# Kernel tuning notes

Hardware: AMD Instinct MI355X
Metric: run time of the kernel (lower is better)

The kernel has to match this reference:

```python
import jax, jax.numpy as jnp
import numpy as np

N = 100000      # nodes
E = 1200000     # edges (avg degree 12)
DIN = 64        # input_dim
HID = 64        # hidden_dim
HEADS = 4
CH = HID // 4   # 16 per-head channels; concat -> HID


def setup_inputs() -> dict:
    key = jax.random.key(0)
    ks = jax.random.split(key, 16)
    s = 0.05
    return {
        "x": jax.random.normal(ks[0], (N, DIN), jnp.float32),
        "edge_index": jax.random.randint(ks[1], (2, E), 0, N, jnp.int32),
        # GCN layers
        "W1": s * jax.random.normal(ks[2], (DIN, HID), jnp.float32),
        "b1": jnp.zeros((HID,), jnp.float32),
        "W2": s * jax.random.normal(ks[3], (HID, HID), jnp.float32),
        "b2": jnp.zeros((HID,), jnp.float32),
        "W3": s * jax.random.normal(ks[4], (HID, HID // 2), jnp.float32),
        "b3": jnp.zeros((HID // 2,), jnp.float32),
        # GAT layer: in = HID//2 = 32, out per head = HID//4 = 16, 4 heads concat -> 64
        "Wg": s * jax.random.normal(ks[5], (HID // 2, HEADS * CH), jnp.float32),
        "att_src": s * jax.random.normal(ks[6], (HEADS, CH), jnp.float32),
        "att_dst": s * jax.random.normal(ks[7], (HEADS, CH), jnp.float32),
        "bg": jnp.zeros((HEADS * CH,), jnp.float32),
        # classifier MLP
        "Wc1": s * jax.random.normal(ks[8], (HID, HID // 2), jnp.float32),
        "bc1": jnp.zeros((HID // 2,), jnp.float32),
        "Wc2": s * jax.random.normal(ks[9], (HID // 2, 2), jnp.float32),
        "bc2": jnp.zeros((2,), jnp.float32),
    }


def reference(x, edge_index, W1, b1, W2, b2, W3, b3,
              Wg, att_src, att_dst, bg, Wc1, bc1, Wc2, bc2):
    n = x.shape[0]
    # add self-loops (PyG default for GCNConv and GATConv)
    loops = jnp.arange(n, dtype=edge_index.dtype)
    src = jnp.concatenate([edge_index[0], loops])
    dst = jnp.concatenate([edge_index[1], loops])

    # symmetric GCN normalization: deg^-1/2[src] * deg^-1/2[dst]
    deg = jax.ops.segment_sum(jnp.ones(src.shape, x.dtype), dst, num_segments=n)
    dinv = jnp.where(deg > 0, jax.lax.rsqrt(deg), 0.0)
    norm = (dinv[src] * dinv[dst])[:, None]  # [E+N, 1]

    def gcn(h, W, b):
        h = h @ W                                   # [N, out]
        msg = h[src] * norm                         # gather + scale, [E+N, out]
        return jax.ops.segment_sum(msg, dst, num_segments=n) + b

    h = jax.nn.relu(gcn(x, W1, b1))   # dropout = identity (eval mode)
    h = jax.nn.relu(gcn(h, W2, b2))
    h = jax.nn.relu(gcn(h, W3, b3))   # [N, HID//2]

    # GATConv, 4 heads, concat
    heads, ch = att_src.shape
    g = (h @ Wg).reshape(n, heads, ch)                       # [N, H, C]
    a_s = jnp.einsum('nhc,hc->nh', g, att_src)               # [N, H]
    a_d = jnp.einsum('nhc,hc->nh', g, att_dst)
    e = jax.nn.leaky_relu(a_s[src] + a_d[dst], 0.2)          # [E+N, H]
    m = jax.ops.segment_max(e, dst, num_segments=n)          # per-dst max
    ex = jnp.exp(e - m[dst])
    den = jax.ops.segment_sum(ex, dst, num_segments=n)
    alpha = ex / den[dst]                                    # segment softmax
    o = jax.ops.segment_sum(g[src] * alpha[:, :, None], dst, num_segments=n)
    o = jax.nn.relu(o.reshape(n, heads * ch) + bg)           # [N, HID]

    pooled = jnp.mean(o, axis=0, keepdims=True)              # batch=None path: [1, HID]
    z = jax.nn.relu(pooled @ Wc1 + bc1)
    return z @ Wc2 + bc2                                     # [1, 2]
```

## Files before the change

kernel.cpp:

```cpp
#include <hip/hip_runtime.h>
#include <hip/hip_bf16.h>
#include <hip/hip_fp16.h>
#include <math.h>

__device__ __forceinline__ unsigned h2u(__half2 h) { return *reinterpret_cast<unsigned*>(&h); }
__device__ __forceinline__ __half2 u2h(unsigned u) { return *reinterpret_cast<__half2*>(&u); }
__device__ __forceinline__ __half2 shfl_h2(__half2 h, int off) {
  int v = __shfl_xor((int)h2u(h), off);
  unsigned uv = (unsigned)v;
  return u2h(uv);
}


#define P1E 16
#define NBK 400

__global__ __launch_bounds__(256) void hist_gemm1(const int* __restrict__ dst,
                                                  int* __restrict__ bcnt, int e,
                                                  int fillBlocks,
                                                  const float* __restrict__ H,
                                                  const float* __restrict__ W,
                                                  unsigned short* __restrict__ T, int n) {
  __shared__ int lcnt[NBK];
  __shared__ float Ws[64 * 64];
  if ((int)blockIdx.x < fillBlocks) {
    for (int i = threadIdx.x; i < NBK; i += 256) lcnt[i] = 0;
    __syncthreads();
    int base = blockIdx.x * (256 * P1E);
#pragma unroll
    for (int r = 0; r < P1E; ++r) {
      int i = base + r * 256 + threadIdx.x;
      if (i < e) atomicAdd(&lcnt[dst[i] >> 8], 1);
    }
    __syncthreads();
    for (int b = threadIdx.x; b < NBK; b += 256)
      if (lcnt[b]) atomicAdd(&bcnt[b], lcnt[b]);
    return;
  }
  for (int idx = threadIdx.x; idx < 64 * 64 / 4; idx += 256)
    reinterpret_cast<float4*>(Ws)[idx] = reinterpret_cast<const float4*>(W)[idx];
  __syncthreads();
  int bid = blockIdx.x - fillBlocks;
  int tx = threadIdx.x % 16;
  int ty = threadIdx.x / 16;
  int j0 = tx * 4;
  int n0 = bid * 32 + ty * 2;
  const float* h0p = H + (size_t)min(n0 + 0, n - 1) * 64;
  const float* h1p = H + (size_t)min(n0 + 1, n - 1) * 64;
  float4 acc0 = {0,0,0,0}, acc1 = {0,0,0,0};
#pragma unroll 2
  for (int k = 0; k < 64; k += 4) {
    float4 ha = *reinterpret_cast<const float4*>(h0p + k);
    float4 hb = *reinterpret_cast<const float4*>(h1p + k);
    float4 w0 = *reinterpret_cast<const float4*>(&Ws[(k + 0) * 64 + j0]);
    float4 w1 = *reinterpret_cast<const float4*>(&Ws[(k + 1) * 64 + j0]);
    float4 w2 = *reinterpret_cast<const float4*>(&Ws[(k + 2) * 64 + j0]);
    float4 w3 = *reinterpret_cast<const float4*>(&Ws[(k + 3) * 64 + j0]);
#define A4(A, HV)                                                                \
    A.x = fmaf(HV.x, w0.x, A.x); A.y = fmaf(HV.x, w0.y, A.y);                    \
    A.z = fmaf(HV.x, w0.z, A.z); A.w = fmaf(HV.x, w0.w, A.w);                    \
    A.x = fmaf(HV.y, w1.x, A.x); A.y = fmaf(HV.y, w1.y, A.y);                    \
    A.z = fmaf(HV.y, w1.z, A.z); A.w = fmaf(HV.y, w1.w, A.w);                    \
    A.x = fmaf(HV.z, w2.x, A.x); A.y = fmaf(HV.z, w2.y, A.y);                    \
    A.z = fmaf(HV.z, w2.z, A.z); A.w = fmaf(HV.z, w2.w, A.w);                    \
    A.x = fmaf(HV.w, w3.x, A.x); A.y = fmaf(HV.w, w3.y, A.y);                    \
    A.z = fmaf(HV.w, w3.z, A.z); A.w = fmaf(HV.w, w3.w, A.w);
    A4(acc0, ha) A4(acc1, hb)
#undef A4
  }
  float4 av[2] = {acc0, acc1};
#pragma unroll
  for (int i = 0; i < 2; ++i) {
    int node = n0 + i;
    if (node < n) {
      uint2 st;
      st.x = h2u(__floats2half2_rn(av[i].x, av[i].y));
      st.y = h2u(__floats2half2_rn(av[i].z, av[i].w));
      *reinterpret_cast<uint2*>(T + (size_t)node * 64 + j0) = st;
    }
  }
}

__global__ __launch_bounds__(512) void bucket_scan(const int* __restrict__ bcnt,
                                                   int* __restrict__ bucket_base,
                                                   int* __restrict__ gcursor,
                                                   int nb, int e) {
  __shared__ int s[512];
  int v = (threadIdx.x < (unsigned)nb) ? bcnt[threadIdx.x] : 0;
  s[threadIdx.x] = v;
  __syncthreads();
  for (int off = 1; off < 512; off <<= 1) {
    int t = (threadIdx.x >= (unsigned)off) ? s[threadIdx.x - off] : 0;
    __syncthreads();
    s[threadIdx.x] += t;
    __syncthreads();
  }
  if (threadIdx.x < (unsigned)nb) {
    int excl = s[threadIdx.x] - v;
    bucket_base[threadIdx.x] = excl;
    gcursor[threadIdx.x] = excl;
  }
  if (threadIdx.x == 0) bucket_base[nb] = e;
}

__global__ __launch_bounds__(256) void bin_pass1(const int* __restrict__ src,
                                                 const int* __restrict__ dst,
                                                 int* __restrict__ gcursor,
                                                 unsigned* __restrict__ stream, int e) {
  __shared__ int lcnt[NBK], gbase[NBK];
  for (int i = threadIdx.x; i < NBK; i += 256) lcnt[i] = 0;
  __syncthreads();
  int base = blockIdx.x * (256 * P1E);
  int rankr[P1E];
#pragma unroll
  for (int r = 0; r < P1E; ++r) {
    int i = base + r * 256 + threadIdx.x;
    rankr[r] = (i < e) ? atomicAdd(&lcnt[dst[i] >> 8], 1) : 0;
  }
  __syncthreads();
  for (int bkt = threadIdx.x; bkt < NBK; bkt += 256)
    gbase[bkt] = lcnt[bkt] ? atomicAdd(&gcursor[bkt], lcnt[bkt]) : 0;
  __syncthreads();
#pragma unroll
  for (int r = 0; r < P1E; ++r) {
    int i = base + r * 256 + threadIdx.x;
    if (i < e) {
      int d = dst[i];
      stream[gbase[d >> 8] + rankr[r]] = ((unsigned)src[i] << 8) | (unsigned)(d & 255);
    }
  }
}


#define LCAP 6144

__global__ __launch_bounds__(256) void bin_pass2(const unsigned* __restrict__ stream,
                                                 const int* __restrict__ bucket_base,
                                                 int* __restrict__ row_start,
                                                 int* __restrict__ cnt,
                                                 int* __restrict__ csr_src,
                                                 int n, int e) {
  __shared__ int lcnt[256];
  __shared__ int lscan[256];
  __shared__ int lcur[256];
  __shared__ int lbuf[LCAP];
  int node_lo = blockIdx.x << 8;
  int nn = min(256, n - node_lo);
  int lo = bucket_base[blockIdx.x];
  int hi = bucket_base[blockIdx.x + 1];
  int sz = hi - lo;
  lcnt[threadIdx.x] = 0;
  __syncthreads();
  for (int j = threadIdx.x; j < sz; j += 256)
    atomicAdd(&lcnt[stream[lo + j] & 255], 1);
  __syncthreads();
  int v = lcnt[threadIdx.x];
  lscan[threadIdx.x] = v;
  __syncthreads();
  for (int off = 1; off < 256; off <<= 1) {
    int t = (threadIdx.x >= (unsigned)off) ? lscan[threadIdx.x - off] : 0;
    __syncthreads();
    lscan[threadIdx.x] += t;
    __syncthreads();
  }
  int excl = lscan[threadIdx.x] - v;
  if ((int)threadIdx.x < nn) {
    row_start[node_lo + threadIdx.x] = lo + excl;
    cnt[node_lo + threadIdx.x] = v;
  }
  if (blockIdx.x == 0 && threadIdx.x == 0) row_start[n] = e;
  lcur[threadIdx.x] = excl;
  __syncthreads();
  if (sz <= LCAP) {
    for (int j = threadIdx.x; j < sz; j += 256) {
      unsigned r = stream[lo + j];
      int slot = atomicAdd(&lcur[r & 255], 1);
      lbuf[slot] = (int)(r >> 8);
    }
    __syncthreads();
    for (int j = threadIdx.x; j < sz; j += 256)
      csr_src[lo + j] = lbuf[j];
  } else {
    for (int j = threadIdx.x; j < sz; j += 256) {
      unsigned r = stream[lo + j];
      int slot = atomicAdd(&lcur[r & 255], 1);
      csr_src[lo + slot] = (int)(r >> 8);
    }
  }
}


template <int IN, int OUT, bool ATT>
__global__ __launch_bounds__(256) void gemm2x4(const unsigned short* __restrict__ Hh,
                                               const float* __restrict__ W,
                                               const float* __restrict__ att_src,
                                               const float* __restrict__ att_dst,
                                               unsigned short* __restrict__ T,
                                               float* __restrict__ a_s,
                                               float* __restrict__ a_d, int n) {
  constexpr int TX = OUT / 4;
  constexpr int NB = (256 / TX) * 2;
  __shared__ float Ws[IN * OUT];
  __shared__ float asv[ATT ? OUT : 1], adv[ATT ? OUT : 1];
  __shared__ float lds_as[ATT ? NB * 4 : 1], lds_ad[ATT ? NB * 4 : 1];

  for (int idx = threadIdx.x; idx < IN * OUT / 4; idx += 256)
    reinterpret_cast<float4*>(Ws)[idx] = reinterpret_cast<const float4*>(W)[idx];
  if (ATT) {
    if (threadIdx.x < OUT) {
      asv[threadIdx.x] = att_src[threadIdx.x];
      adv[threadIdx.x] = att_dst[threadIdx.x];
    }
    for (int idx = threadIdx.x; idx < NB * 4; idx += 256) {
      lds_as[idx] = 0.f; lds_ad[idx] = 0.f;
    }
  }
  __syncthreads();

  int tx = threadIdx.x % TX;
  int ty = threadIdx.x / TX;
  int j0 = tx * 4;
  int base = blockIdx.x * NB;
  int n0 = base + ty * 2;

  const unsigned short* h0p = Hh + (size_t)min(n0 + 0, n - 1) * IN;
  const unsigned short* h1p = Hh + (size_t)min(n0 + 1, n - 1) * IN;

  float4 acc0 = {0,0,0,0}, acc1 = {0,0,0,0};
#pragma unroll 2
  for (int k = 0; k < IN; k += 4) {
    uint2 va = *reinterpret_cast<const uint2*>(h0p + k);
    uint2 vb = *reinterpret_cast<const uint2*>(h1p + k);
    float2 a01 = __half22float2(u2h(va.x)), a23 = __half22float2(u2h(va.y));
    float2 b01 = __half22float2(u2h(vb.x)), b23 = __half22float2(u2h(vb.y));
    float4 ha = {a01.x, a01.y, a23.x, a23.y};
    float4 hb = {b01.x, b01.y, b23.x, b23.y};
    float4 w0 = *reinterpret_cast<const float4*>(&Ws[(k + 0) * OUT + j0]);
    float4 w1 = *reinterpret_cast<const float4*>(&Ws[(k + 1) * OUT + j0]);
    float4 w2 = *reinterpret_cast<const float4*>(&Ws[(k + 2) * OUT + j0]);
    float4 w3 = *reinterpret_cast<const float4*>(&Ws[(k + 3) * OUT + j0]);
#define A4(A, HV)                                                                \
    A.x = fmaf(HV.x, w0.x, A.x); A.y = fmaf(HV.x, w0.y, A.y);                    \
    A.z = fmaf(HV.x, w0.z, A.z); A.w = fmaf(HV.x, w0.w, A.w);                    \
    A.x = fmaf(HV.y, w1.x, A.x); A.y = fmaf(HV.y, w1.y, A.y);                    \
    A.z = fmaf(HV.y, w1.z, A.z); A.w = fmaf(HV.y, w1.w, A.w);                    \
    A.x = fmaf(HV.z, w2.x, A.x); A.y = fmaf(HV.z, w2.y, A.y);                    \
    A.z = fmaf(HV.z, w2.z, A.z); A.w = fmaf(HV.z, w2.w, A.w);                    \
    A.x = fmaf(HV.w, w3.x, A.x); A.y = fmaf(HV.w, w3.y, A.y);                    \
    A.z = fmaf(HV.w, w3.z, A.z); A.w = fmaf(HV.w, w3.w, A.w);
    A4(acc0, ha) A4(acc1, hb)
#undef A4
  }

  float4 av[2] = {acc0, acc1};
#pragma unroll
  for (int i = 0; i < 2; ++i) {
    int node = n0 + i;
    if (node < n) {
      float o0 = av[i].x, o1 = av[i].y, o2 = av[i].z, o3 = av[i].w;
      uint2 st;
      st.x = h2u(__floats2half2_rn(o0, o1));
      st.y = h2u(__floats2half2_rn(o2, o3));
      *reinterpret_cast<uint2*>(T + (size_t)node * OUT + j0) = st;
      if (ATT) {
        int head = tx >> 2;
        float cs = o0 * asv[j0] + o1 * asv[j0 + 1] + o2 * asv[j0 + 2] + o3 * asv[j0 + 3];
        float cd = o0 * adv[j0] + o1 * adv[j0 + 1] + o2 * adv[j0 + 2] + o3 * adv[j0 + 3];
        atomicAdd(&lds_as[(ty * 2 + i) * 4 + head], cs);
        atomicAdd(&lds_ad[(ty * 2 + i) * 4 + head], cd);
      }
    }
  }
  if (ATT) {
    __syncthreads();
    for (int idx = threadIdx.x; idx < NB * 4; idx += 256) {
      int node = base + (idx >> 2);
      if (node < n) {
        a_s[(size_t)base * 4 + idx] = lds_as[idx];
        a_d[(size_t)base * 4 + idx] = lds_ad[idx];
      }
    }
  }
}


template <int C, bool DINV, bool PRE>
__global__ __launch_bounds__(256) void gcn_agg(const unsigned short* __restrict__ T,
                                               const int* __restrict__ row_start,
                                               const int* __restrict__ csr_src,
                                               const int* __restrict__ cnt,
                                               const float* __restrict__ b,
                                               unsigned short* __restrict__ out, int n) {
  constexpr int LPR = C / 8;
  constexpr int SLOTS = 64 / LPR;
  constexpr unsigned RS4 = C / 8;
  int wid = threadIdx.x >> 6;
  int lane = threadIdx.x & 63;
  int node = blockIdx.x * 4 + wid;
  if (node >= n) return;
  int q = lane & (LPR - 1);
  int g = lane / LPR;
  const uint4* Tp = reinterpret_cast<const uint4*>(T);
  int rs = row_start[node], re = row_start[node + 1];
  float dn = rsqrtf((float)(cnt[node] + 1));
  __half2 A0 = u2h(0u), A1 = u2h(0u), A2 = u2h(0u), A3 = u2h(0u);
  if (g == 0) {
    uint4 v = Tp[(unsigned)node * RS4 + q];
    if constexpr (DINV) {
      __half2 hw = __float2half2_rn(dn);
      A0 = __hmul2(hw, u2h(v.x)); A1 = __hmul2(hw, u2h(v.y));
      A2 = __hmul2(hw, u2h(v.z)); A3 = __hmul2(hw, u2h(v.w));
    } else {
      A0 = u2h(v.x); A1 = u2h(v.y); A2 = u2h(v.z); A3 = u2h(v.w);
    }
  }
  if constexpr (C == 64) {
    __half2 B0 = u2h(0u), B1 = u2h(0u), B2 = u2h(0u), B3 = u2h(0u);
    int i = rs + g;
    while (i < re) {
      bool v2 = (i + 8) < re;
      unsigned s1 = (unsigned)csr_src[i];
      unsigned s2 = v2 ? (unsigned)csr_src[i + 8] : s1;
      uint4 r1 = Tp[s1 * RS4 + q];
      uint4 r2 = Tp[s2 * RS4 + q];
      if constexpr (DINV) {
        float w1f = rsqrtf((float)(cnt[s1] + 1));
        float w2f = v2 ? rsqrtf((float)(cnt[s2] + 1)) : 0.f;
        __half2 hw1 = __float2half2_rn(w1f);
        __half2 hw2 = __float2half2_rn(w2f);
        A0 = __hfma2(hw1, u2h(r1.x), A0); A1 = __hfma2(hw1, u2h(r1.y), A1);
        A2 = __hfma2(hw1, u2h(r1.z), A2); A3 = __hfma2(hw1, u2h(r1.w), A3);
        B0 = __hfma2(hw2, u2h(r2.x), B0); B1 = __hfma2(hw2, u2h(r2.y), B1);
        B2 = __hfma2(hw2, u2h(r2.z), B2); B3 = __hfma2(hw2, u2h(r2.w), B3);
      } else {
        if (!v2) { r2.x = 0u; r2.y = 0u; r2.z = 0u; r2.w = 0u; }
        A0 = __hadd2(A0, u2h(r1.x)); A1 = __hadd2(A1, u2h(r1.y));
        A2 = __hadd2(A2, u2h(r1.z)); A3 = __hadd2(A3, u2h(r1.w));
        B0 = __hadd2(B0, u2h(r2.x)); B1 = __hadd2(B1, u2h(r2.y));
        B2 = __hadd2(B2, u2h(r2.z)); B3 = __hadd2(B3, u2h(r2.w));
      }
      i += 16;
    }
    A0 = __hadd2(A0, B0); A1 = __hadd2(A1, B1);
    A2 = __hadd2(A2, B2); A3 = __hadd2(A3, B3);
  } else {
    for (int i = rs + g; i < re; i += SLOTS) {
      unsigned s = (unsigned)csr_src[i];
      uint4 v = Tp[s * RS4 + q];
      A0 = __hadd2(A0, u2h(v.x)); A1 = __hadd2(A1, u2h(v.y));
      A2 = __hadd2(A2, u2h(v.z)); A3 = __hadd2(A3, u2h(v.w));
    }
  }
#pragma unroll
  for (int off = LPR; off < 64; off <<= 1) {
    A0 = __hadd2(A0, shfl_h2(A0, off));
    A1 = __hadd2(A1, shfl_h2(A1, off));
    A2 = __hadd2(A2, shfl_h2(A2, off));
    A3 = __hadd2(A3, shfl_h2(A3, off));
  }
  if (lane < LPR) {
    float4 b0 = *reinterpret_cast<const float4*>(b + 8 * q);
    float4 b1 = *reinterpret_cast<const float4*>(b + 8 * q + 4);
    float2 f0 = __half22float2(A0), f1 = __half22float2(A1);
    float2 f2 = __half22float2(A2), f3 = __half22float2(A3);
    float sc = PRE ? dn : 1.f;
    float r0 = sc * fmaxf(fmaf(dn, f0.x, b0.x), 0.f);
    float r1 = sc * fmaxf(fmaf(dn, f0.y, b0.y), 0.f);
    float r2 = sc * fmaxf(fmaf(dn, f1.x, b0.z), 0.f);
    float r3 = sc * fmaxf(fmaf(dn, f1.y, b0.w), 0.f);
    float r4 = sc * fmaxf(fmaf(dn, f2.x, b1.x), 0.f);
    float r5 = sc * fmaxf(fmaf(dn, f2.y, b1.y), 0.f);
    float r6 = sc * fmaxf(fmaf(dn, f3.x, b1.z), 0.f);
    float r7 = sc * fmaxf(fmaf(dn, f3.y, b1.w), 0.f);
    uint4 o;
    o.x = h2u(__floats2half2_rn(r0, r1));
    o.y = h2u(__floats2half2_rn(r2, r3));
    o.z = h2u(__floats2half2_rn(r4, r5));
    o.w = h2u(__floats2half2_rn(r6, r7));
    reinterpret_cast<uint4*>(out)[(unsigned)node * RS4 + q] = o;
  }
}


__device__ __forceinline__ float lrelu(float v) { return v > 0.f ? v : 0.2f * v; }

__global__ __launch_bounds__(256) void gat_agg(const unsigned short* __restrict__ g,
                                               const float* __restrict__ a_s,
                                               const float* __restrict__ a_d,
                                               const int* __restrict__ row_start,
                                               const int* __restrict__ csr_src,
                                               const float* __restrict__ bg,
                                               float* __restrict__ partial1, int n) {
  __shared__ float pacc[4][64];
  int wid = threadIdx.x >> 6;
  int lane = threadIdx.x & 63;
  int node = blockIdx.x * 4 + wid;
  bool active = node < n;
  int q = lane & 7;
  int gslot = lane >> 3;
  int h = q >> 1;
  const uint4* gp = reinterpret_cast<const uint4*>(g);
  int rs = 0, re = 0;
  float ad_h = 0.f;
  if (active) {
    rs = row_start[node];
    re = row_start[node + 1];
    ad_h = a_d[(unsigned)node * 4u + h];
  }
  float den = 0.f, den2 = 0.f;
  __half2 A0 = u2h(0u), A1 = u2h(0u), A2 = u2h(0u), A3 = u2h(0u);
  __half2 C0 = u2h(0u), C1 = u2h(0u), C2 = u2h(0u), C3 = u2h(0u);
  if (active && gslot == 0) {
    float w = __expf(lrelu(a_s[(unsigned)node * 4u + h] + ad_h));
    uint4 v = gp[(unsigned)node * 8u + q];
    den = w;
    __half2 w2 = __float2half2_rn(w);
    A0 = __hmul2(w2, u2h(v.x)); A1 = __hmul2(w2, u2h(v.y));
    A2 = __hmul2(w2, u2h(v.z)); A3 = __hmul2(w2, u2h(v.w));
  }
  int i = rs + gslot;
  while (i < re) {
    bool v2 = (i + 8) < re;
    unsigned s1 = (unsigned)csr_src[i];
    unsigned s2 = v2 ? (unsigned)csr_src[i + 8] : s1;
    float e1 = a_s[s1 * 4u + h];
    float e2 = a_s[s2 * 4u + h];
    uint4 r1 = gp[s1 * 8u + q];
    uint4 r2 = gp[s2 * 8u + q];
    float w1 = __expf(lrelu(e1 + ad_h));
    float w2 = v2 ? __expf(lrelu(e2 + ad_h)) : 0.f;
    den += w1;
    den2 += w2;
    __half2 hw1 = __float2half2_rn(w1);
    __half2 hw2 = __float2half2_rn(w2);
    A0 = __hfma2(hw1, u2h(r1.x), A0); A1 = __hfma2(hw1, u2h(r1.y), A1);
    A2 = __hfma2(hw1, u2h(r1.z), A2); A3 = __hfma2(hw1, u2h(r1.w), A3);
    C0 = __hfma2(hw2, u2h(r2.x), C0); C1 = __hfma2(hw2, u2h(r2.y), C1);
    C2 = __hfma2(hw2, u2h(r2.z), C2); C3 = __hfma2(hw2, u2h(r2.w), C3);
    i += 16;
  }
  den += den2;
  A0 = __hadd2(A0, C0); A1 = __hadd2(A1, C1);
  A2 = __hadd2(A2, C2); A3 = __hadd2(A3, C3);
#pragma unroll
  for (int off = 8; off < 64; off <<= 1) {
    den += __shfl_xor(den, off);
    A0 = __hadd2(A0, shfl_h2(A0, off));
    A1 = __hadd2(A1, shfl_h2(A1, off));
    A2 = __hadd2(A2, shfl_h2(A2, off));
    A3 = __hadd2(A3, shfl_h2(A3, off));
  }
  if (lane < 8) {
    float inv = active ? (1.f / den) : 0.f;
    float4 b0 = *reinterpret_cast<const float4*>(bg + 8 * q);
    float4 b1 = *reinterpret_cast<const float4*>(bg + 8 * q + 4);
    float2 f0 = __half22float2(A0), f1 = __half22float2(A1);
    float2 f2 = __half22float2(A2), f3 = __half22float2(A3);
    int c0 = 8 * q;
    pacc[wid][c0 + 0] = active ? fmaxf(fmaf(f0.x, inv, b0.x), 0.f) : 0.f;
    pacc[wid][c0 + 1] = active ? fmaxf(fmaf(f0.y, inv, b0.y), 0.f) : 0.f;
    pacc[wid][c0 + 2] = active ? fmaxf(fmaf(f1.x, inv, b0.z), 0.f) : 0.f;
    pacc[wid][c0 + 3] = active ? fmaxf(fmaf(f1.y, inv, b0.w), 0.f) : 0.f;
    pacc[wid][c0 + 4] = active ? fmaxf(fmaf(f2.x, inv, b1.x), 0.f) : 0.f;
    pacc[wid][c0 + 5] = active ? fmaxf(fmaf(f2.y, inv, b1.y), 0.f) : 0.f;
    pacc[wid][c0 + 6] = active ? fmaxf(fmaf(f3.x, inv, b1.z), 0.f) : 0.f;
    pacc[wid][c0 + 7] = active ? fmaxf(fmaf(f3.y, inv, b1.w), 0.f) : 0.f;
  }
  __syncthreads();
  if (threadIdx.x < 64) {
    int t = threadIdx.x;
    partial1[(size_t)blockIdx.x * 64 + t] =
        pacc[0][t] + pacc[1][t] + pacc[2][t] + pacc[3][t];
  }
}


#define PBLK 512

__global__ __launch_bounds__(256) void pool_partial(const float* __restrict__ P1,
                                                    double* __restrict__ partial2,
                                                    unsigned total) {
  unsigned tid = blockIdx.x * 256u + threadIdx.x;
  unsigned stride = PBLK * 256u;
  double a = 0.0;
  for (unsigned i = tid; i < total; i += stride) a += (double)P1[i];
  __shared__ double red[256];
  red[threadIdx.x] = a;
  __syncthreads();
  if (threadIdx.x < 64) {
    int t = threadIdx.x;
    double s = red[t] + red[t + 64] + red[t + 128] + red[t + 192];
    partial2[(size_t)blockIdx.x * 64 + t] = s;
  }
}

__global__ __launch_bounds__(64) void final_kernel(const double* __restrict__ partial, int nblocks,
                                                   const float* __restrict__ Wc1,
                                                   const float* __restrict__ bc1,
                                                   const float* __restrict__ Wc2,
                                                   const float* __restrict__ bc2,
                                                   float* __restrict__ out, int n) {
  __shared__ float pooled[64];
  __shared__ float z[32];
  int t = threadIdx.x;
  double s = 0.0;
#pragma unroll 4
  for (int b = 0; b < nblocks; ++b) s += partial[(size_t)b * 64 + t];
  pooled[t] = (float)(s / (double)n);
  __syncthreads();
  if (t < 32) {
    double a = 0.0;
    for (int k = 0; k < 64; ++k) a += (double)pooled[k] * (double)Wc1[k * 32 + t];
    z[t] = fmaxf((float)a + bc1[t], 0.f);
  }
  __syncthreads();
  if (t < 2) {
    double a = 0.0;
    for (int j = 0; j < 32; ++j) a += (double)z[j] * (double)Wc2[j * 2 + t];
    out[t] = (float)a + bc2[t];
  }
}


extern "C" void kernel_launch(void* const* d_in, const int* in_sizes, int n_in,
                              void* d_out, int out_size, void* d_ws, size_t ws_size,
                              hipStream_t stream) {
  const float* x   = (const float*)d_in[0];
  const int* eidx  = (const int*)d_in[1];
  const float* W1  = (const float*)d_in[2];
  const float* b1  = (const float*)d_in[3];
  const float* W2  = (const float*)d_in[4];
  const float* b2  = (const float*)d_in[5];
  const float* W3  = (const float*)d_in[6];
  const float* b3  = (const float*)d_in[7];
  const float* Wg  = (const float*)d_in[8];
  const float* att_src = (const float*)d_in[9];
  const float* att_dst = (const float*)d_in[10];
  const float* bg  = (const float*)d_in[11];
  const float* Wc1 = (const float*)d_in[12];
  const float* bc1 = (const float*)d_in[13];
  const float* Wc2 = (const float*)d_in[14];
  const float* bc2 = (const float*)d_in[15];

  const int n = in_sizes[0] / 64;
  const int e = in_sizes[1] / 2;
  const int* src = eidx;
  const int* dst = eidx + e;

  char* ws = (char*)d_ws;
  size_t off = 0;
  auto alloc = [&](size_t bytes) {
    void* p = ws + off;
    off += (bytes + 255) & ~(size_t)255;
    return p;
  };
  const int nbuckets = (n + 255) >> 8;
  const int nblk4 = (n + 3) / 4;
  int*      cnt        = (int*)alloc((size_t)n * 4);
  int*      row_start  = (int*)alloc(((size_t)n + 1) * 4);
  unsigned* stream_b   = (unsigned*)alloc((size_t)e * 4);
  int*      csr_src    = (int*)alloc((size_t)e * 4);
  int*      bcnt       = (int*)alloc(NBK * 4);
  int*      bucket_base = (int*)alloc((NBK + 1) * 4);
  int*      gcursor    = (int*)alloc(NBK * 4);
  unsigned short* bufT = (unsigned short*)alloc((size_t)n * 64 * 2);
  unsigned short* bufF = (unsigned short*)alloc((size_t)n * 64 * 2);
  float*    a_s        = (float*)alloc((size_t)n * 4 * 4);
  float*    a_d        = (float*)alloc((size_t)n * 4 * 4);
  float*    partial1   = (float*)alloc((size_t)nblk4 * 64 * 4);
  double*   partial2   = (double*)alloc((size_t)PBLK * 64 * 8);

  hipMemsetAsync(bcnt, 0, NBK * 4, stream);

  int g64 = (n + 31) / 32;
  int g32 = (n + 63) / 64;
  int p1blk = (e + 256 * P1E - 1) / (256 * P1E);

  hist_gemm1<<<p1blk + g64, 256, 0, stream>>>(dst, bcnt, e, p1blk, x, W1, bufT, n);
  bucket_scan<<<1, 512, 0, stream>>>(bcnt, bucket_base, gcursor, nbuckets, e);
  bin_pass1<<<p1blk, 256, 0, stream>>>(src, dst, gcursor, stream_b, e);
  bin_pass2<<<nbuckets, 256, 0, stream>>>(stream_b, bucket_base, row_start, cnt,
                                          csr_src, n, e);

  gcn_agg<64, true, true><<<nblk4, 256, 0, stream>>>(bufT, row_start, csr_src, cnt, b1, bufF, n);
  gemm2x4<64, 64, false><<<g64, 256, 0, stream>>>(bufF, W2, nullptr, nullptr,
                                                  bufT, nullptr, nullptr, n);
  gcn_agg<64, false, true><<<nblk4, 256, 0, stream>>>(bufT, row_start, csr_src, cnt, b2, bufF, n);
  gemm2x4<64, 32, false><<<g32, 256, 0, stream>>>(bufF, W3, nullptr, nullptr,
                                                  bufT, nullptr, nullptr, n);
  gcn_agg<32, false, false><<<nblk4, 256, 0, stream>>>(bufT, row_start, csr_src, cnt, b3, bufF, n);
  gemm2x4<32, 64, true><<<g64, 256, 0, stream>>>(bufF, Wg, att_src, att_dst,
                                                 bufT, a_s, a_d, n);
  gat_agg<<<nblk4, 256, 0, stream>>>(bufT, a_s, a_d, row_start, csr_src, bg, partial1, n);
  pool_partial<<<PBLK, 256, 0, stream>>>(partial1, partial2, (unsigned)nblk4 * 64u);
  final_kernel<<<1, 64, 0, stream>>>(partial2, PBLK, Wc1, bc1, Wc2, bc2, (float*)d_out, n);
}
```

Measured before the change: 315.6 us.

## Fuse GCN aggregation with following dense GEMM in one kernel

Merges each gcn_agg pass with the next layer's weight multiply (and the GAT attention-score computation) into one 1024-thread kernel. Each block aggregates 16 nodes into shared memory, then multiplies by the weight matrix held in shared memory. This removes three launches and the round trip of the aggregated features through global memory. In exchange, each block reloads the full weight matrix, uses a scalar per-output GEMM, and the larger blocks may lower occupancy.

```diff
diff --git a/kernel.cpp b/kernel.cpp
--- a/kernel.cpp
+++ b/kernel.cpp
@@ -131,7 +131,6 @@
   }
 }
 
-
 #define LCAP 6144
 
 __global__ __launch_bounds__(256) void bin_pass2(const unsigned* __restrict__ stream,
@@ -190,121 +189,51 @@
 }
 
 
-template <int IN, int OUT, bool ATT>
-__global__ __launch_bounds__(256) void gemm2x4(const unsigned short* __restrict__ Hh,
-                                               const float* __restrict__ W,
-                                               const float* __restrict__ att_src,
-                                               const float* __restrict__ att_dst,
-                                               unsigned short* __restrict__ T,
-                                               float* __restrict__ a_s,
-                                               float* __restrict__ a_d, int n) {
-  constexpr int TX = OUT / 4;
-  constexpr int NB = (256 / TX) * 2;
-  __shared__ float Ws[IN * OUT];
-  __shared__ float asv[ATT ? OUT : 1], adv[ATT ? OUT : 1];
-  __shared__ float lds_as[ATT ? NB * 4 : 1], lds_ad[ATT ? NB * 4 : 1];
-
-  for (int idx = threadIdx.x; idx < IN * OUT / 4; idx += 256)
+__device__ __forceinline__ float lrelu(float v) { return v > 0.f ? v : 0.2f * v; }
+
+template <int CIN, int COUT, bool DINV, bool ATT, bool SCO>
+__global__ __launch_bounds__(1024) void gcn_gemm(const unsigned short* __restrict__ T,
+                                                 const int* __restrict__ row_start,
+                                                 const int* __restrict__ csr_src,
+                                                 const int* __restrict__ cnt,
+                                                 const float* __restrict__ b,
+                                                 const float* __restrict__ W,
+                                                 const float* __restrict__ att_src,
+                                                 const float* __restrict__ att_dst,
+                                                 unsigned short* __restrict__ Tout,
+                                                 float* __restrict__ a_s,
+                                                 float* __restrict__ a_d, int n) {
+  constexpr int LPR = CIN / 8;
+  constexpr unsigned RS4 = CIN / 8;
+  __shared__ float Ws[CIN * COUT];
+  __shared__ float hrow[16][CIN];
+  __shared__ float asv[ATT ? COUT : 1], adv[ATT ? COUT : 1];
+
+  for (int idx = threadIdx.x; idx < CIN * COUT / 4; idx += 1024)
     reinterpret_cast<float4*>(Ws)[idx] = reinterpret_cast<const float4*>(W)[idx];
   if (ATT) {
-    if (threadIdx.x < OUT) {
+    if (threadIdx.x < COUT) {
       asv[threadIdx.x] = att_src[threadIdx.x];
       adv[threadIdx.x] = att_dst[threadIdx.x];
     }
-    for (int idx = threadIdx.x; idx < NB * 4; idx += 256) {
-      lds_as[idx] = 0.f; lds_ad[idx] = 0.f;
-    }
-  }
-  __syncthreads();
-
-  int tx = threadIdx.x % TX;
-  int ty = threadIdx.x / TX;
-  int j0 = tx * 4;
-  int base = blockIdx.x * NB;
-  int n0 = base + ty * 2;
-
-  const unsigned short* h0p = Hh + (size_t)min(n0 + 0, n - 1) * IN;
-  const unsigned short* h1p = Hh + (size_t)min(n0 + 1, n - 1) * IN;
-
-  float4 acc0 = {0,0,0,0}, acc1 = {0,0,0,0};
-#pragma unroll 2
-  for (int k = 0; k < IN; k += 4) {
-    uint2 va = *reinterpret_cast<const uint2*>(h0p + k);
-    uint2 vb = *reinterpret_cast<const uint2*>(h1p + k);
-    float2 a01 = __half22float2(u2h(va.x)), a23 = __half22float2(u2h(va.y));
-    float2 b01 = __half22float2(u2h(vb.x)), b23 = __half22float2(u2h(vb.y));
-    float4 ha = {a01.x, a01.y, a23.x, a23.y};
-    float4 hb = {b01.x, b01.y, b23.x, b23.y};
-    float4 w0 = *reinterpret_cast<const float4*>(&Ws[(k + 0) * OUT + j0]);
-    float4 w1 = *reinterpret_cast<const float4*>(&Ws[(k + 1) * OUT + j0]);
-    float4 w2 = *reinterpret_cast<const float4*>(&Ws[(k + 2) * OUT + j0]);
-    float4 w3 = *reinterpret_cast<const float4*>(&Ws[(k + 3) * OUT + j0]);
-#define A4(A, HV)                                                                \
-    A.x = fmaf(HV.x, w0.x, A.x); A.y = fmaf(HV.x, w0.y, A.y);                    \
-    A.z = fmaf(HV.x, w0.z, A.z); A.w = fmaf(HV.x, w0.w, A.w);                    \
-    A.x = fmaf(HV.y, w1.x, A.x); A.y = fmaf(HV.y, w1.y, A.y);                    \
-    A.z = fmaf(HV.y, w1.z, A.z); A.w = fmaf(HV.y, w1.w, A.w);                    \
-    A.x = fmaf(HV.z, w2.x, A.x); A.y = fmaf(HV.z, w2.y, A.y);                    \
-    A.z = fmaf(HV.z, w2.z, A.z); A.w = fmaf(HV.z, w2.w, A.w);                    \
-    A.x = fmaf(HV.w, w3.x, A.x); A.y = fmaf(HV.w, w3.y, A.y);                    \
-    A.z = fmaf(HV.w, w3.z, A.z); A.w = fmaf(HV.w, w3.w, A.w);
-    A4(acc0, ha) A4(acc1, hb)
-#undef A4
-  }
-
-  float4 av[2] = {acc0, acc1};
-#pragma unroll
-  for (int i = 0; i < 2; ++i) {
-    int node = n0 + i;
-    if (node < n) {
-      float o0 = av[i].x, o1 = av[i].y, o2 = av[i].z, o3 = av[i].w;
-      uint2 st;
-      st.x = h2u(__floats2half2_rn(o0, o1));
-      st.y = h2u(__floats2half2_rn(o2, o3));
-      *reinterpret_cast<uint2*>(T + (size_t)node * OUT + j0) = st;
-      if (ATT) {
-        int head = tx >> 2;
-        float cs = o0 * asv[j0] + o1 * asv[j0 + 1] + o2 * asv[j0 + 2] + o3 * asv[j0 + 3];
-        float cd = o0 * adv[j0] + o1 * adv[j0 + 1] + o2 * adv[j0 + 2] + o3 * adv[j0 + 3];
-        atomicAdd(&lds_as[(ty * 2 + i) * 4 + head], cs);
-        atomicAdd(&lds_ad[(ty * 2 + i) * 4 + head], cd);
-      }
-    }
-  }
-  if (ATT) {
-    __syncthreads();
-    for (int idx = threadIdx.x; idx < NB * 4; idx += 256) {
-      int node = base + (idx >> 2);
-      if (node < n) {
-        a_s[(size_t)base * 4 + idx] = lds_as[idx];
-        a_d[(size_t)base * 4 + idx] = lds_ad[idx];
-      }
-    }
-  }
-}
-
-
-template <int C, bool DINV, bool PRE>
-__global__ __launch_bounds__(256) void gcn_agg(const unsigned short* __restrict__ T,
-                                               const int* __restrict__ row_start,
-                                               const int* __restrict__ csr_src,
-                                               const int* __restrict__ cnt,
-                                               const float* __restrict__ b,
-                                               unsigned short* __restrict__ out, int n) {
-  constexpr int LPR = C / 8;
-  constexpr int SLOTS = 64 / LPR;
-  constexpr unsigned RS4 = C / 8;
+  }
+
   int wid = threadIdx.x >> 6;
   int lane = threadIdx.x & 63;
-  int node = blockIdx.x * 4 + wid;
-  if (node >= n) return;
+  int node = blockIdx.x * 16 + wid;
+  bool active = node < n;
   int q = lane & (LPR - 1);
   int g = lane / LPR;
   const uint4* Tp = reinterpret_cast<const uint4*>(T);
-  int rs = row_start[node], re = row_start[node + 1];
-  float dn = rsqrtf((float)(cnt[node] + 1));
+  int rs = 0, re = 0;
+  float dn = 1.f;
+  if (active) {
+    rs = row_start[node];
+    re = row_start[node + 1];
+    dn = rsqrtf((float)(cnt[node] + 1));
+  }
   __half2 A0 = u2h(0u), A1 = u2h(0u), A2 = u2h(0u), A3 = u2h(0u);
-  if (g == 0) {
+  if (active && g == 0) {
     uint4 v = Tp[(unsigned)node * RS4 + q];
     if constexpr (DINV) {
       __half2 hw = __float2half2_rn(dn);
@@ -314,7 +243,7 @@
       A0 = u2h(v.x); A1 = u2h(v.y); A2 = u2h(v.z); A3 = u2h(v.w);
     }
   }
-  if constexpr (C == 64) {
+  if constexpr (CIN == 64) {
     __half2 B0 = u2h(0u), B1 = u2h(0u), B2 = u2h(0u), B3 = u2h(0u);
     int i = rs + g;
     while (i < re) {
@@ -344,7 +273,7 @@
     A0 = __hadd2(A0, B0); A1 = __hadd2(A1, B1);
     A2 = __hadd2(A2, B2); A3 = __hadd2(A3, B3);
   } else {
-    for (int i = rs + g; i < re; i += SLOTS) {
+    for (int i = rs + g; i < re; i += 16) {
       unsigned s = (unsigned)csr_src[i];
       uint4 v = Tp[s * RS4 + q];
       A0 = __hadd2(A0, u2h(v.x)); A1 = __hadd2(A1, u2h(v.y));
@@ -363,26 +292,56 @@
     float4 b1 = *reinterpret_cast<const float4*>(b + 8 * q + 4);
     float2 f0 = __half22float2(A0), f1 = __half22float2(A1);
     float2 f2 = __half22float2(A2), f3 = __half22float2(A3);
-    float sc = PRE ? dn : 1.f;
-    float r0 = sc * fmaxf(fmaf(dn, f0.x, b0.x), 0.f);
-    float r1 = sc * fmaxf(fmaf(dn, f0.y, b0.y), 0.f);
-    float r2 = sc * fmaxf(fmaf(dn, f1.x, b0.z), 0.f);
-    float r3 = sc * fmaxf(fmaf(dn, f1.y, b0.w), 0.f);
-    float r4 = sc * fmaxf(fmaf(dn, f2.x, b1.x), 0.f);
-    float r5 = sc * fmaxf(fmaf(dn, f2.y, b1.y), 0.f);
-    float r6 = sc * fmaxf(fmaf(dn, f3.x, b1.z), 0.f);
-    float r7 = sc * fmaxf(fmaf(dn, f3.y, b1.w), 0.f);
-    uint4 o;
-    o.x = h2u(__floats2half2_rn(r0, r1));
-    o.y = h2u(__floats2half2_rn(r2, r3));
-    o.z = h2u(__floats2half2_rn(r4, r5));
-    o.w = h2u(__floats2half2_rn(r6, r7));
-    reinterpret_cast<uint4*>(out)[(unsigned)node * RS4 + q] = o;
-  }
-}
-
-
-__device__ __forceinline__ float lrelu(float v) { return v > 0.f ? v : 0.2f * v; }
+    int c0 = 8 * q;
+    hrow[wid][c0 + 0] = fmaxf(fmaf(dn, f0.x, b0.x), 0.f);
+    hrow[wid][c0 + 1] = fmaxf(fmaf(dn, f0.y, b0.y), 0.f);
+    hrow[wid][c0 + 2] = fmaxf(fmaf(dn, f1.x, b0.z), 0.f);
+    hrow[wid][c0 + 3] = fmaxf(fmaf(dn, f1.y, b0.w), 0.f);
+    hrow[wid][c0 + 4] = fmaxf(fmaf(dn, f2.x, b1.x), 0.f);
+    hrow[wid][c0 + 5] = fmaxf(fmaf(dn, f2.y, b1.y), 0.f);
+    hrow[wid][c0 + 6] = fmaxf(fmaf(dn, f3.x, b1.z), 0.f);
+    hrow[wid][c0 + 7] = fmaxf(fmaf(dn, f3.y, b1.w), 0.f);
+  }
+  __syncthreads();
+
+  int nd, j;
+  if constexpr (COUT == 64) { nd = threadIdx.x >> 6; j = threadIdx.x & 63; }
+  else { nd = threadIdx.x >> 5; j = threadIdx.x & 31; }
+  if (nd < 16) {
+    int onode = blockIdx.x * 16 + nd;
+    float acc = 0.f;
+#pragma unroll 8
+    for (int k = 0; k < CIN; k += 4) {
+      float4 hv = *reinterpret_cast<const float4*>(&hrow[nd][k]);
+      acc = fmaf(hv.x, Ws[(k + 0) * COUT + j], acc);
+      acc = fmaf(hv.y, Ws[(k + 1) * COUT + j], acc);
+      acc = fmaf(hv.z, Ws[(k + 2) * COUT + j], acc);
+      acc = fmaf(hv.w, Ws[(k + 3) * COUT + j], acc);
+    }
+    bool ost = onode < n;
+    if (ost) {
+      float sc = 1.f;
+      if constexpr (SCO) sc = rsqrtf((float)(cnt[onode] + 1));
+      __half hv = __float2half(acc * sc);
+      if (ost) Tout[(size_t)onode * COUT + j] = *reinterpret_cast<unsigned short*>(&hv);
+    }
+    if constexpr (ATT) {
+      float cs = acc * asv[j];
+      float cd = acc * adv[j];
+#pragma unroll
+      for (int off = 1; off < 16; off <<= 1) {
+        cs += __shfl_xor(cs, off);
+        cd += __shfl_xor(cd, off);
+      }
+      if (ost && (j & 15) == 0) {
+        int head = j >> 4;
+        a_s[(unsigned)onode * 4u + head] = cs;
+        a_d[(unsigned)onode * 4u + head] = cd;
+      }
+    }
+  }
+}
+
 
 __global__ __launch_bounds__(256) void gat_agg(const unsigned short* __restrict__ g,
                                                const float* __restrict__ a_s,
@@ -556,6 +515,7 @@
   };
   const int nbuckets = (n + 255) >> 8;
   const int nblk4 = (n + 3) / 4;
+  const int nblk16 = (n + 15) / 16;
   int*      cnt        = (int*)alloc((size_t)n * 4);
   int*      row_start  = (int*)alloc(((size_t)n + 1) * 4);
   unsigned* stream_b   = (unsigned*)alloc((size_t)e * 4);
@@ -573,7 +533,6 @@
   hipMemsetAsync(bcnt, 0, NBK * 4, stream);
 
   int g64 = (n + 31) / 32;
-  int g32 = (n + 63) / 64;
   int p1blk = (e + 256 * P1E - 1) / (256 * P1E);
 
   hist_gemm1<<<p1blk + g64, 256, 0, stream>>>(dst, bcnt, e, p1blk, x, W1, bufT, n);
@@ -582,16 +541,13 @@
   bin_pass2<<<nbuckets, 256, 0, stream>>>(stream_b, bucket_base, row_start, cnt,
                                           csr_src, n, e);
 
-  gcn_agg<64, true, true><<<nblk4, 256, 0, stream>>>(bufT, row_start, csr_src, cnt, b1, bufF, n);
-  gemm2x4<64, 64, false><<<g64, 256, 0, stream>>>(bufF, W2, nullptr, nullptr,
-                                                  bufT, nullptr, nullptr, n);
-  gcn_agg<64, false, true><<<nblk4, 256, 0, stream>>>(bufT, row_start, csr_src, cnt, b2, bufF, n);
-  gemm2x4<64, 32, false><<<g32, 256, 0, stream>>>(bufF, W3, nullptr, nullptr,
-                                                  bufT, nullptr, nullptr, n);
-  gcn_agg<32, false, false><<<nblk4, 256, 0, stream>>>(bufT, row_start, csr_src, cnt, b3, bufF, n);
-  gemm2x4<32, 64, true><<<g64, 256, 0, stream>>>(bufF, Wg, att_src, att_dst,
-                                                 bufT, a_s, a_d, n);
-  gat_agg<<<nblk4, 256, 0, stream>>>(bufT, a_s, a_d, row_start, csr_src, bg, partial1, n);
+  gcn_gemm<64, 64, true, false, true><<<nblk16, 1024, 0, stream>>>(
+      bufT, row_start, csr_src, cnt, b1, W2, nullptr, nullptr, bufF, nullptr, nullptr, n);
+  gcn_gemm<64, 32, false, false, true><<<nblk16, 1024, 0, stream>>>(
+      bufF, row_start, csr_src, cnt, b2, W3, nullptr, nullptr, bufT, nullptr, nullptr, n);
+  gcn_gemm<32, 64, false, true, false><<<nblk16, 1024, 0, stream>>>(
+      bufT, row_start, csr_src, cnt, b3, Wg, att_src, att_dst, bufF, a_s, a_d, n);
+  gat_agg<<<nblk4, 256, 0, stream>>>(bufF, a_s, a_d, row_start, csr_src, bg, partial1, n);
   pool_partial<<<PBLK, 256, 0, stream>>>(partial1, partial2, (unsigned)nblk4 * 64u);
   final_kernel<<<1, 64, 0, stream>>>(partial2, PBLK, Wc1, bc1, Wc2, bc2, (float*)d_out, n);
 }
```

After: 355.8 us. 12.7% more time.
